# Optimization experiments

Measured on AMD Instinct MI355X. Metric: run time of the kernel, lower is better.

The kernel has to match this reference:

```python
import jax, jax.numpy as jnp
import numpy as np

B, T, C = 2, 2048, 512
H = 16
HS = C // H  # 32
DF = 4 * C   # 2048
EPS = 1e-3   # keras LayerNormalization default


def setup_inputs() -> dict:
    key = jax.random.key(0)
    ks = jax.random.split(key, 16)
    s = 0.02
    return {
        "x":  jax.random.normal(ks[0], (B, T, C), jnp.float32),
        "Wq": jax.random.normal(ks[1], (H, C, HS), jnp.float32) * s,
        "bq": jnp.zeros((H, HS), jnp.float32),
        "Wk": jax.random.normal(ks[2], (H, C, HS), jnp.float32) * s,
        "bk": jnp.zeros((H, HS), jnp.float32),
        "Wv": jax.random.normal(ks[3], (H, C, HS), jnp.float32) * s,
        "bv": jnp.zeros((H, HS), jnp.float32),
        "Wo": jax.random.normal(ks[4], (C, C), jnp.float32) * s,
        "bo": jnp.zeros((C,), jnp.float32),
        "W1": jax.random.normal(ks[5], (C, DF), jnp.float32) * s,
        "b1": jnp.zeros((DF,), jnp.float32),
        "W2": jax.random.normal(ks[6], (DF, C), jnp.float32) * s,
        "b2": jnp.zeros((C,), jnp.float32),
        "g1": jnp.ones((C,), jnp.float32),
        "be1": jnp.zeros((C,), jnp.float32),
        "g2": jnp.ones((C,), jnp.float32),
        "be2": jnp.zeros((C,), jnp.float32),
    }


def _layernorm(x, g, b):
    mu = jnp.mean(x, axis=-1, keepdims=True)
    var = jnp.mean(jnp.square(x - mu), axis=-1, keepdims=True)
    return (x - mu) / jnp.sqrt(var + EPS) * g + b


def reference(x, Wq, bq, Wk, bk, Wv, bv, Wo, bo, W1, b1, W2, b2, g1, be1, g2, be2):
    Bx, Tx, Cx = x.shape
    # --- attention branch (pre-LN) ---
    h = _layernorm(x, g1, be1)
    q = jnp.einsum('btc,hcd->bhtd', h, Wq) + bq[None, :, None, :]
    k = jnp.einsum('btc,hcd->bhtd', h, Wk) + bk[None, :, None, :]
    v = jnp.einsum('btc,hcd->bhtd', h, Wv) + bv[None, :, None, :]
    # NOTE: source code never applies 1/sqrt(head_size) to scores (mask-only scaling bug)
    scores = jnp.einsum('bhtd,bhsd->bhts', q, k)           # [B,H,T,T]
    causal = jnp.tril(jnp.ones((Tx, Tx), dtype=bool))
    scores = jnp.where(causal, scores, -jnp.inf)
    att = jax.nn.softmax(scores, axis=-1)
    o = jnp.einsum('bhts,bhsd->bhtd', att, v)              # [B,H,T,HS]
    o = o.transpose(0, 2, 1, 3).reshape(Bx, Tx, Cx)        # concat heads
    x = x + o @ Wo + bo
    # --- FFN branch (pre-LN) ---
    h2 = _layernorm(x, g2, be2)
    f = jax.nn.relu(h2 @ W1 + b1) @ W2 + b2
    return x + f
```

## Files before the change

kernel.cpp:

```cpp
#include <hip/hip_runtime.h>
#include <hip/hip_bf16.h>

#define T_  2048
#define C_  512
#define H_  16
#define HS_ 32
#define DF_ 2048
#define B_  2
#define M_  4096

typedef __attribute__((ext_vector_type(8))) short short8;
typedef __attribute__((ext_vector_type(4))) short short4v;
typedef __attribute__((ext_vector_type(4))) float f32x4;
typedef __attribute__((ext_vector_type(16))) float f32x16;

__device__ inline short bf16r(float f) {
  union { float f; unsigned u; } v; v.f = f;
  return (short)((v.u + 0x7FFFu + ((v.u >> 16) & 1u)) >> 16);
}

__device__ inline f32x4 mfma16(short8 a, short8 b, f32x4 c) {
  return __builtin_amdgcn_mfma_f32_16x16x32_bf16(a, b, c, 0, 0, 0);
}
__device__ inline f32x16 mfma32(short8 a, short8 b, f32x16 c) {
  return __builtin_amdgcn_mfma_f32_32x32x16_bf16(a, b, c, 0, 0, 0);
}

__device__ inline unsigned cvtpk(float lo, float hi) {
  unsigned r;
  asm("v_cvt_pk_bf16_f32 %0, %1, %2" : "=v"(r) : "v"(lo), "v"(hi));
  return r;
}

__device__ inline void gload_lds16(const short* g, short* l) {
  __builtin_amdgcn_global_load_lds(
      (const __attribute__((address_space(1))) unsigned int*)g,
      (__attribute__((address_space(3))) unsigned int*)l, 16, 0, 0);
}

__device__ inline void ln_row(int row, const float* src, const float* g,
                              const float* be, short* dst, int lane) {
  const float* xr = src + (size_t)row * C_;
  float4 a = *(const float4*)(xr + lane * 8);
  float4 b = *(const float4*)(xr + lane * 8 + 4);
  float vals[8] = {a.x, a.y, a.z, a.w, b.x, b.y, b.z, b.w};
  float s = 0.f, ss = 0.f;
  #pragma unroll
  for (int i = 0; i < 8; ++i) { s += vals[i]; ss += vals[i] * vals[i]; }
  #pragma unroll
  for (int off = 1; off < 64; off <<= 1) {
    s += __shfl_xor(s, off);
    ss += __shfl_xor(ss, off);
  }
  float mu = s * (1.f / C_);
  float rstd = rsqrtf(ss * (1.f / C_) - mu * mu + 1e-3f);
  short8 o;
  #pragma unroll
  for (int i = 0; i < 8; ++i)
    o[i] = bf16r((vals[i] - mu) * rstd * g[lane * 8 + i] + be[lane * 8 + i]);
  *(short8*)(dst + (size_t)row * C_ + lane * 8) = o;
}

__global__ __launch_bounds__(256) void prep_kernel(
    const float* __restrict__ x, const float* __restrict__ g1, const float* __restrict__ be1,
    const float* __restrict__ Wq, const float* __restrict__ Wk, const float* __restrict__ Wv,
    const float* __restrict__ Wo, const float* __restrict__ W1, const float* __restrict__ W2,
    short* __restrict__ h1, short* __restrict__ Wqkv, short* __restrict__ Wop,
    short* __restrict__ W1p, short* __restrict__ W2p) {
  __shared__ float tile[32][33];
  int id = blockIdx.x;
  int tid = threadIdx.x;
  if (id >= 3072) {
    int w = tid >> 6, lane = tid & 63;
    ln_row((id - 3072) * 4 + w, x, g1, be1, h1, lane);
    return;
  }
  const float* src; short* dst;
  int srcN, dstK, k0, n0;
  size_t dstBase;
  if (id < 768) {
    int s = id >> 4, ct = id & 15;
    int proj = s >> 4, hh = s & 15;
    src = (proj == 0 ? Wq : (proj == 1 ? Wk : Wv)) + (size_t)hh * 512 * 32;
    srcN = 32; dstK = 512; k0 = ct * 32; n0 = 0;
    dst = Wqkv; dstBase = (size_t)(proj * 512 + hh * 32);
  } else if (id < 1024) {
    int t = id - 768;
    src = Wo; srcN = 512; dstK = 512;
    k0 = (t >> 4) * 32; n0 = (t & 15) * 32; dst = Wop; dstBase = 0;
  } else if (id < 2048) {
    int t = id - 1024;
    src = W1; srcN = 2048; dstK = 512;
    k0 = (t >> 6) * 32; n0 = (t & 63) * 32; dst = W1p; dstBase = 0;
  } else {
    int t = id - 2048;
    src = W2; srcN = 512; dstK = 2048;
    k0 = (t >> 4) * 32; n0 = (t & 15) * 32; dst = W2p; dstBase = 0;
  }
  int rr = tid >> 3, rc = (tid & 7) * 4;
  float4 v4 = *(const float4*)(src + (size_t)(k0 + rr) * srcN + n0 + rc);
  tile[rr][rc + 0] = v4.x; tile[rr][rc + 1] = v4.y;
  tile[rr][rc + 2] = v4.z; tile[rr][rc + 3] = v4.w;
  __syncthreads();
  int wn = tid >> 3, wk = (tid & 7) * 4;
  short4v o;
  o[0] = bf16r(tile[wk + 0][wn]);
  o[1] = bf16r(tile[wk + 1][wn]);
  o[2] = bf16r(tile[wk + 2][wn]);
  o[3] = bf16r(tile[wk + 3][wn]);
  *(short4v*)(dst + (dstBase + n0 + wn) * (size_t)dstK + k0 + wk) = o;
}

__global__ __launch_bounds__(256) void ln2_kernel(
    const float* __restrict__ x, const float* __restrict__ g, const float* __restrict__ be,
    short* __restrict__ out) {
  int w = threadIdx.x >> 6, lane = threadIdx.x & 63;
  ln_row(blockIdx.x * 4 + w, x, g, be, out, lane);
}

template<int BM, int BN, int WM, int WN, int KDIM, int FM, int FN>
__device__ inline void gemm_core(const short* __restrict__ A, const short* __restrict__ Bw,
                                 int m0, int n0, f32x4 (&acc)[FM][FN]) {
  static_assert(WM * WN == 4 && FM == BM / WM / 16 && FN == BN / WN / 16, "geometry");
  __shared__ short lA[2][BM * 64];
  __shared__ short lB[2][BN * 64];
  const int tid = threadIdx.x, w = tid >> 6, lane = tid & 63;
  const int cl = lane & 15, g = lane >> 4;
  const int wm = w / WN, wn = w % WN;
  const int srow = tid >> 3;
  const int sug  = (tid & 7) ^ (srow & 7);
  constexpr int NT = KDIM / 64;

  auto stage = [&](int buf, int k0) {
    #pragma unroll
    for (int j = 0; j < BM / 32; ++j)
      gload_lds16(A + (size_t)(m0 + j * 32 + srow) * KDIM + k0 + sug * 8,
                  &lA[buf][j * 2048 + tid * 8]);
    #pragma unroll
    for (int j = 0; j < BN / 32; ++j)
      gload_lds16(Bw + (size_t)(n0 + j * 32 + srow) * KDIM + k0 + sug * 8,
                  &lB[buf][j * 2048 + tid * 8]);
  };

  stage(0, 0);
  __syncthreads();
  int cur = 0;
  for (int t = 0; t < NT; ++t) {
    if (t + 1 < NT) stage(cur ^ 1, (t + 1) * 64);
    #pragma unroll
    for (int kk = 0; kk < 2; ++kk) {
      const int uswz = ((kk * 4 + g) ^ (cl & 7)) * 8;
      short8 a[FM], b[FN];
      #pragma unroll
      for (int mi = 0; mi < FM; ++mi)
        a[mi] = *(const short8*)&lA[cur][(wm * (BM / WM) + mi * 16 + cl) * 64 + uswz];
      #pragma unroll
      for (int ni = 0; ni < FN; ++ni)
        b[ni] = *(const short8*)&lB[cur][(wn * (BN / WN) + ni * 16 + cl) * 64 + uswz];
      #pragma unroll
      for (int mi = 0; mi < FM; ++mi)
        #pragma unroll
        for (int ni = 0; ni < FN; ++ni)
          acc[mi][ni] = mfma16(a[mi], b[ni], acc[mi][ni]);
    }
    __syncthreads();
    cur ^= 1;
  }
}

__global__ __launch_bounds__(256) void gemm_qkvt(
    const short* __restrict__ h1, const short* __restrict__ Wqkv,
    const float* __restrict__ bq, const float* __restrict__ bk,
    const float* __restrict__ bv,
    short* __restrict__ qb, short* __restrict__ kb, short* __restrict__ vTb) {
  int id = blockIdx.x;
  const short *Ap, *Bp;
  int m0, n0;
  bool isv = id >= 512;
  if (!isv) { m0 = (id >> 3) * 64; n0 = (id & 7) * 128; Ap = h1; Bp = Wqkv; }
  else { int t = id - 512; m0 = (t & 7) * 64; n0 = (t >> 3) * 128;
         Ap = Wqkv + 1024 * 512; Bp = h1; }
  f32x4 acc[2][4] = {};
  gemm_core<64, 128, 2, 2, 512, 2, 4>(Ap, Bp, m0, n0, acc);
  int w = threadIdx.x >> 6, lane = threadIdx.x & 63;
  int cl = lane & 15, rb = (lane >> 4) * 4;
  int wm = w >> 1, wn = w & 1;
  if (!isv) {
    #pragma unroll
    for (int mi = 0; mi < 2; ++mi)
      #pragma unroll
      for (int ni = 0; ni < 4; ++ni)
        #pragma unroll
        for (int r = 0; r < 4; ++r) {
          int mm = m0 + wm * 32 + mi * 16 + rb + r;
          int n  = n0 + wn * 64 + ni * 16 + cl;
          int proj = n >> 9, rem = n & 511;
          int hh = rem >> 5, d = rem & 31;
          int b = mm >> 11, t = mm & (T_ - 1);
          size_t bh = (size_t)b * H_ + hh;
          float val = acc[mi][ni][r];
          if (proj == 0) qb[(bh * T_ + t) * HS_ + d] = bf16r(val + bq[rem]);
          else           kb[(bh * T_ + t) * HS_ + d] = bf16r(val + bk[rem]);
        }
  } else {
    #pragma unroll
    for (int mi = 0; mi < 2; ++mi)
      #pragma unroll
      for (int ni = 0; ni < 4; ++ni)
        #pragma unroll
        for (int r = 0; r < 4; ++r) {
          int m = m0 + wm * 32 + mi * 16 + rb + r;
          int n = n0 + wn * 64 + ni * 16 + cl;
          vTb[(size_t)(n >> 11) * (512 * 2048) + (size_t)m * T_ + (n & 2047)] =
              bf16r(acc[mi][ni][r] + bv[m]);
        }
  }
}

__global__ __launch_bounds__(256) void gemm_ffn1(
    const short* __restrict__ A, const short* __restrict__ W,
    const float* __restrict__ b1, short* __restrict__ f1) {
  int id = blockIdx.x;
  int xcd = id & 7, s = id >> 3;
  int m0 = (xcd * 8 + (s & 7)) * 64;
  int n0 = (s >> 3) * 128;
  f32x4 acc[2][4] = {};
  gemm_core<64, 128, 2, 2, 512, 2, 4>(A, W, m0, n0, acc);
  int w = threadIdx.x >> 6, lane = threadIdx.x & 63;
  int cl = lane & 15, rb = (lane >> 4) * 4;
  int wm = w >> 1, wn = w & 1;
  #pragma unroll
  for (int mi = 0; mi < 2; ++mi)
    #pragma unroll
    for (int ni = 0; ni < 4; ++ni)
      #pragma unroll
      for (int r = 0; r < 4; ++r) {
        int mm = m0 + wm * 32 + mi * 16 + rb + r;
        int n  = n0 + wn * 64 + ni * 16 + cl;
        f1[(size_t)mm * DF_ + n] = bf16r(fmaxf(acc[mi][ni][r] + b1[n], 0.f));
      }
}

template<int KDIM>
__global__ __launch_bounds__(256) void gemm_res(
    const short* __restrict__ A, const short* __restrict__ W,
    const float* __restrict__ bias, const float* __restrict__ res,
    float* __restrict__ dst) {
  __shared__ short lA[2][64 * 128];
  __shared__ short lB[2][64 * 128];
  int id = blockIdx.x;
  int xcd = id & 7, s = id >> 3;
  int m0 = (xcd * 8 + (s & 7)) * 64;
  int n0 = (s >> 3) * 64;
  const int tid = threadIdx.x, w = tid >> 6, lane = tid & 63;
  const int cl = lane & 15, g = lane >> 4;
  const int wm = w >> 1, wn = w & 1;
  const int srow16 = tid >> 4;
  const int sug = (tid & 15) ^ (srow16 & 7);
  constexpr int NT = KDIM / 128;
  f32x4 acc[2][2] = {};

  auto stage = [&](int buf, int k0) {
    #pragma unroll
    for (int j = 0; j < 4; ++j) {
      gload_lds16(A + (size_t)(m0 + j * 16 + srow16) * KDIM + k0 + sug * 8,
                  &lA[buf][j * 2048 + tid * 8]);
      gload_lds16(W + (size_t)(n0 + j * 16 + srow16) * KDIM + k0 + sug * 8,
                  &lB[buf][j * 2048 + tid * 8]);
    }
  };

  stage(0, 0);
  __syncthreads();
  int cur = 0;
  for (int t = 0; t < NT; ++t) {
    if (t + 1 < NT) stage(cur ^ 1, (t + 1) * 128);
    #pragma unroll
    for (int kk = 0; kk < 4; ++kk) {
      const int uswz = ((kk * 4 + g) ^ (cl & 7)) * 8;
      short8 a0 = *(const short8*)&lA[cur][(wm * 32 + cl) * 128 + uswz];
      short8 a1 = *(const short8*)&lA[cur][(wm * 32 + 16 + cl) * 128 + uswz];
      short8 b0 = *(const short8*)&lB[cur][(wn * 32 + cl) * 128 + uswz];
      short8 b1 = *(const short8*)&lB[cur][(wn * 32 + 16 + cl) * 128 + uswz];
      acc[0][0] = mfma16(a0, b0, acc[0][0]);
      acc[0][1] = mfma16(a0, b1, acc[0][1]);
      acc[1][0] = mfma16(a1, b0, acc[1][0]);
      acc[1][1] = mfma16(a1, b1, acc[1][1]);
    }
    __syncthreads();
    cur ^= 1;
  }

  int rb = (lane >> 4) * 4;
  #pragma unroll
  for (int mi = 0; mi < 2; ++mi)
    #pragma unroll
    for (int ni = 0; ni < 2; ++ni)
      #pragma unroll
      for (int r = 0; r < 4; ++r) {
        int mm = m0 + wm * 32 + mi * 16 + rb + r;
        int n  = n0 + wn * 32 + ni * 16 + cl;
        dst[(size_t)mm * C_ + n] = acc[mi][ni][r] + bias[n] + res[(size_t)mm * C_ + n];
      }
}

__global__ __launch_bounds__(256) void attn_kernel(
    const short* __restrict__ qb, const short* __restrict__ kb,
    const short* __restrict__ vTb, short* __restrict__ ob) {
  __shared__ float accbuf[4][64][17];
  __shared__ float lbuf[4][32];
  __shared__ short tbuf[32][34];
  const int id = blockIdx.x;
  const int xcd = id & 7, s = id >> 3;
  const int headin = s & 3;
  const int qt = 63 - (s >> 2);
  const int bh = xcd * 4 + headin;
  const int w = threadIdx.x >> 6, lane = threadIdx.x & 63;
  const int cl = lane & 31, g = lane >> 5;
  const int q0 = qt * 32, q = q0 + cl;
  const float L2E = 1.44269504f;
  const float NFM = -16.f * L2E;

  const short* Qp  = qb  + (size_t)bh * T_ * HS_;
  const short* Kp  = kb  + (size_t)bh * T_ * HS_;
  const short* VTp = vTb + (size_t)bh * HS_ * T_;

  const int nc   = (qt >> 1) + 1;
  const int cbeg = (nc * w) >> 2;
  const int cend = (nc * (w + 1)) >> 2;

  f32x16 acc = {};
  float l = 0.f;

  if (cbeg < cend) {
    short8 qf0 = *(const short8*)(Qp + (size_t)q * HS_ + g * 8);
    short8 qf1 = *(const short8*)(Qp + (size_t)q * HS_ + 16 + g * 8);

    for (int c = cbeg; c < cend; ++c) {
      const int kc = c << 6;
      short8 k00 = *(const short8*)(Kp + (size_t)(kc + cl) * HS_ + g * 8);
      short8 k01 = *(const short8*)(Kp + (size_t)(kc + cl) * HS_ + 16 + g * 8);
      short8 k10 = *(const short8*)(Kp + (size_t)(kc + 32 + cl) * HS_ + g * 8);
      short8 k11 = *(const short8*)(Kp + (size_t)(kc + 32 + cl) * HS_ + 16 + g * 8);
      short8 va = *(const short8*)(VTp + (size_t)cl * T_ + kc + g * 8);
      short8 vb = *(const short8*)(VTp + (size_t)cl * T_ + kc + 16 + g * 8);
      short8 vc = *(const short8*)(VTp + (size_t)cl * T_ + kc + 32 + g * 8);
      short8 vd = *(const short8*)(VTp + (size_t)cl * T_ + kc + 48 + g * 8);

      __builtin_amdgcn_s_setprio(1);
      f32x16 Z = {};
      f32x16 S0 = mfma32(k00, qf0, Z);
      S0 = mfma32(k01, qf1, S0);
      f32x16 S1 = mfma32(k10, qf0, Z);
      S1 = mfma32(k11, qf1, S1);
      __builtin_amdgcn_s_setprio(0);

      if (c == nc - 1) {
        #pragma unroll
        for (int r = 0; r < 16; ++r) {
          int key = kc + (r & 3) + 8 * (r >> 2) + 4 * g;
          if (key > q)      S0[r] = -1e30f;
          if (key + 32 > q) S1[r] = -1e30f;
        }
      }

      float p[32];
      #pragma unroll
      for (int r = 0; r < 16; ++r) {
        p[r]      = exp2f(fmaf(S0[r], L2E, NFM));
        p[16 + r] = exp2f(fmaf(S1[r], L2E, NFM));
      }
      float sm[8];
      #pragma unroll
      for (int r = 0; r < 8; ++r)
        sm[r] = (p[r] + p[r + 8]) + (p[16 + r] + p[24 + r]);
      #pragma unroll
      for (int r = 0; r < 4; ++r) sm[r] += sm[r + 4];
      float ps = (sm[0] + sm[1]) + (sm[2] + sm[3]);
      ps += __shfl_xor(ps, 32);
      l += ps;

      __builtin_amdgcn_s_setprio(1);
      #pragma unroll
      for (int sb = 0; sb < 4; ++sb) {
        unsigned L0 = cvtpk(p[sb * 8 + 0], p[sb * 8 + 1]);
        unsigned L1 = cvtpk(p[sb * 8 + 2], p[sb * 8 + 3]);
        unsigned H0 = cvtpk(p[sb * 8 + 4], p[sb * 8 + 5]);
        unsigned H1 = cvtpk(p[sb * 8 + 6], p[sb * 8 + 7]);
        auto r02 = __builtin_amdgcn_permlane32_swap(L0, H0, false, false);
        auto r13 = __builtin_amdgcn_permlane32_swap(L1, H1, false, false);
        union { unsigned u[4]; short8 v; } pb;
        pb.u[0] = r02[0]; pb.u[1] = r13[0]; pb.u[2] = r02[1]; pb.u[3] = r13[1];
        short8 vf = (sb == 0) ? va : (sb == 1) ? vb : (sb == 2) ? vc : vd;
        acc = mfma32(vf, pb.v, acc);
      }
      __builtin_amdgcn_s_setprio(0);
    }
  }

  #pragma unroll
  for (int r = 0; r < 16; ++r) accbuf[w][lane][r] = acc[r];
  if (lane < 32) lbuf[w][cl] = l;
  __syncthreads();

  if (w == 0) {
    float lsum = lbuf[0][cl] + lbuf[1][cl] + lbuf[2][cl] + lbuf[3][cl];
    float inv = 1.f / lsum;
    #pragma unroll
    for (int r = 0; r < 16; ++r) {
      float v = accbuf[0][lane][r] + accbuf[1][lane][r] +
                accbuf[2][lane][r] + accbuf[3][lane][r];
      int d = (r & 3) + 8 * (r >> 2) + 4 * g;
      tbuf[cl][d] = bf16r(v * inv);
    }
  }
  __syncthreads();

  int qr = threadIdx.x >> 3, col = (threadIdx.x & 7) * 4;
  const int b = bh >> 4, hh = bh & 15;
  short4v o4;
  o4[0] = tbuf[qr][col + 0];
  o4[1] = tbuf[qr][col + 1];
  o4[2] = tbuf[qr][col + 2];
  o4[3] = tbuf[qr][col + 3];
  *(short4v*)(ob + ((size_t)b * T_ + q0 + qr) * C_ + hh * HS_ + col) = o4;
}

#define OFF_H1   ((size_t)0)
#define OFF_WQKV ((size_t)4194304)
#define OFF_WO   ((size_t)5767168)
#define OFF_W1   ((size_t)6291456)
#define OFF_W2   ((size_t)8388608)
#define OFF_Q    ((size_t)10485760)
#define OFF_K    ((size_t)14680064)
#define OFF_VT   ((size_t)18874368)
#define OFF_O    ((size_t)23068672)
#define OFF_X1   ((size_t)27262976)
#define OFF_H2   ((size_t)35651584)
#define OFF_F1   ((size_t)39845888)

extern "C" void kernel_launch(void* const* d_in, const int* in_sizes, int n_in,
                              void* d_out, int out_size, void* d_ws, size_t ws_size,
                              hipStream_t stream) {
  const float* x   = (const float*)d_in[0];
  const float* Wq  = (const float*)d_in[1];
  const float* bq  = (const float*)d_in[2];
  const float* Wk  = (const float*)d_in[3];
  const float* bk  = (const float*)d_in[4];
  const float* Wv  = (const float*)d_in[5];
  const float* bv  = (const float*)d_in[6];
  const float* Wo  = (const float*)d_in[7];
  const float* bo  = (const float*)d_in[8];
  const float* W1  = (const float*)d_in[9];
  const float* b1  = (const float*)d_in[10];
  const float* W2  = (const float*)d_in[11];
  const float* b2  = (const float*)d_in[12];
  const float* g1  = (const float*)d_in[13];
  const float* be1 = (const float*)d_in[14];
  const float* g2  = (const float*)d_in[15];
  const float* be2 = (const float*)d_in[16];

  char* ws = (char*)d_ws;
  short* h1   = (short*)(ws + OFF_H1);
  short* Wqkv = (short*)(ws + OFF_WQKV);
  short* Wop  = (short*)(ws + OFF_WO);
  short* W1p  = (short*)(ws + OFF_W1);
  short* W2p  = (short*)(ws + OFF_W2);
  short* qb   = (short*)(ws + OFF_Q);
  short* kb   = (short*)(ws + OFF_K);
  short* vTb  = (short*)(ws + OFF_VT);
  short* ob   = (short*)(ws + OFF_O);
  float* x1   = (float*)(ws + OFF_X1);
  short* h2   = (short*)(ws + OFF_H2);
  short* f1   = (short*)(ws + OFF_F1);
  float* out  = (float*)d_out;

  prep_kernel<<<3072 + 1024, 256, 0, stream>>>(x, g1, be1, Wq, Wk, Wv, Wo, W1, W2,
                                               h1, Wqkv, Wop, W1p, W2p);
  gemm_qkvt<<<768, 256, 0, stream>>>(h1, Wqkv, bq, bk, bv, qb, kb, vTb);
  attn_kernel<<<2048, 256, 0, stream>>>(qb, kb, vTb, ob);
  gemm_res<512><<<512, 256, 0, stream>>>(ob, Wop, bo, x, x1);
  ln2_kernel<<<M_ / 4, 256, 0, stream>>>(x1, g2, be2, h2);
  gemm_ffn1<<<1024, 256, 0, stream>>>(h2, W1p, b1, f1);
  gemm_res<2048><<<512, 256, 0, stream>>>(f1, W2p, b2, x1, out);
}
```

Measured before the change: 103.3 us.

## Split-K the FFN2 GEMM with atomic accumulation into pre-initialized output

The second FFN GEMM (K=2048) is split four ways along K, running 2048 blocks instead of 512, and each block atomically adds its partial tile into the output. The LN2 kernel now also writes out = x1 + b2 so the atomics start from the residual plus bias. The goal is to fill more CUs in the last GEMM. In exchange it adds float atomic traffic and makes the summation order nondeterministic.

```diff
diff --git a/kernel.cpp b/kernel.cpp
--- a/kernel.cpp
+++ b/kernel.cpp
@@ -112,10 +112,37 @@
 }
 
 __global__ __launch_bounds__(256) void ln2_kernel(
-    const float* __restrict__ x, const float* __restrict__ g, const float* __restrict__ be,
-    short* __restrict__ out) {
+    const float* __restrict__ x1, const float* __restrict__ g, const float* __restrict__ be,
+    const float* __restrict__ b2, short* __restrict__ h2, float* __restrict__ outinit) {
   int w = threadIdx.x >> 6, lane = threadIdx.x & 63;
-  ln_row(blockIdx.x * 4 + w, x, g, be, out, lane);
+  int row = blockIdx.x * 4 + w;
+  const float* xr = x1 + (size_t)row * C_;
+  float4 a = *(const float4*)(xr + lane * 8);
+  float4 b = *(const float4*)(xr + lane * 8 + 4);
+  float vals[8] = {a.x, a.y, a.z, a.w, b.x, b.y, b.z, b.w};
+  float s = 0.f, ss = 0.f;
+  #pragma unroll
+  for (int i = 0; i < 8; ++i) { s += vals[i]; ss += vals[i] * vals[i]; }
+  #pragma unroll
+  for (int off = 1; off < 64; off <<= 1) {
+    s += __shfl_xor(s, off);
+    ss += __shfl_xor(ss, off);
+  }
+  float mu = s * (1.f / C_);
+  float rstd = rsqrtf(ss * (1.f / C_) - mu * mu + 1e-3f);
+  short8 o;
+  float4 i0, i1;
+  const float* b2p = b2 + lane * 8;
+  #pragma unroll
+  for (int i = 0; i < 8; ++i)
+    o[i] = bf16r((vals[i] - mu) * rstd * g[lane * 8 + i] + be[lane * 8 + i]);
+  i0.x = vals[0] + b2p[0]; i0.y = vals[1] + b2p[1];
+  i0.z = vals[2] + b2p[2]; i0.w = vals[3] + b2p[3];
+  i1.x = vals[4] + b2p[4]; i1.y = vals[5] + b2p[5];
+  i1.z = vals[6] + b2p[6]; i1.w = vals[7] + b2p[7];
+  *(short8*)(h2 + (size_t)row * C_ + lane * 8) = o;
+  *(float4*)(outinit + (size_t)row * C_ + lane * 8) = i0;
+  *(float4*)(outinit + (size_t)row * C_ + lane * 8 + 4) = i1;
 }
 
 template<int BM, int BN, int WM, int WN, int KDIM, int FM, int FN>
@@ -301,6 +328,69 @@
         int mm = m0 + wm * 32 + mi * 16 + rb + r;
         int n  = n0 + wn * 32 + ni * 16 + cl;
         dst[(size_t)mm * C_ + n] = acc[mi][ni][r] + bias[n] + res[(size_t)mm * C_ + n];
+      }
+}
+
+__global__ __launch_bounds__(256) void gemm_ffn2_sk(
+    const short* __restrict__ A, const short* __restrict__ W,
+    float* __restrict__ out) {
+  __shared__ short lA[2][64 * 128];
+  __shared__ short lB[2][64 * 128];
+  int id = blockIdx.x;
+  int xcd = id & 7, r2 = id >> 3;
+  int ks = r2 & 3, s = r2 >> 2;
+  int m0 = (xcd * 8 + (s & 7)) * 64;
+  int n0 = (s >> 3) * 64;
+  int kbase = ks * 512;
+  const int tid = threadIdx.x, w = tid >> 6, lane = tid & 63;
+  const int cl = lane & 15, g = lane >> 4;
+  const int wm = w >> 1, wn = w & 1;
+  const int srow16 = tid >> 4;
+  const int sug = (tid & 15) ^ (srow16 & 7);
+  constexpr int NT = 4;
+  f32x4 acc[2][2] = {};
+
+  auto stage = [&](int buf, int k0) {
+    #pragma unroll
+    for (int j = 0; j < 4; ++j) {
+      gload_lds16(A + (size_t)(m0 + j * 16 + srow16) * DF_ + kbase + k0 + sug * 8,
+                  &lA[buf][j * 2048 + tid * 8]);
+      gload_lds16(W + (size_t)(n0 + j * 16 + srow16) * DF_ + kbase + k0 + sug * 8,
+                  &lB[buf][j * 2048 + tid * 8]);
+    }
+  };
+
+  stage(0, 0);
+  __syncthreads();
+  int cur = 0;
+  for (int t = 0; t < NT; ++t) {
+    if (t + 1 < NT) stage(cur ^ 1, (t + 1) * 128);
+    #pragma unroll
+    for (int kk = 0; kk < 4; ++kk) {
+      const int uswz = ((kk * 4 + g) ^ (cl & 7)) * 8;
+      short8 a0 = *(const short8*)&lA[cur][(wm * 32 + cl) * 128 + uswz];
+      short8 a1 = *(const short8*)&lA[cur][(wm * 32 + 16 + cl) * 128 + uswz];
+      short8 b0 = *(const short8*)&lB[cur][(wn * 32 + cl) * 128 + uswz];
+      short8 b1 = *(const short8*)&lB[cur][(wn * 32 + 16 + cl) * 128 + uswz];
+      acc[0][0] = mfma16(a0, b0, acc[0][0]);
+      acc[0][1] = mfma16(a0, b1, acc[0][1]);
+      acc[1][0] = mfma16(a1, b0, acc[1][0]);
+      acc[1][1] = mfma16(a1, b1, acc[1][1]);
+    }
+    __syncthreads();
+    cur ^= 1;
+  }
+
+  int rb = (lane >> 4) * 4;
+  #pragma unroll
+  for (int mi = 0; mi < 2; ++mi)
+    #pragma unroll
+    for (int ni = 0; ni < 2; ++ni)
+      #pragma unroll
+      for (int r = 0; r < 4; ++r) {
+        int mm = m0 + wm * 32 + mi * 16 + rb + r;
+        int n  = n0 + wn * 32 + ni * 16 + cl;
+        atomicAdd(&out[(size_t)mm * C_ + n], acc[mi][ni][r]);
       }
 }
 
@@ -480,7 +570,7 @@
   gemm_qkvt<<<768, 256, 0, stream>>>(h1, Wqkv, bq, bk, bv, qb, kb, vTb);
   attn_kernel<<<2048, 256, 0, stream>>>(qb, kb, vTb, ob);
   gemm_res<512><<<512, 256, 0, stream>>>(ob, Wop, bo, x, x1);
-  ln2_kernel<<<M_ / 4, 256, 0, stream>>>(x1, g2, be2, h2);
+  ln2_kernel<<<M_ / 4, 256, 0, stream>>>(x1, g2, be2, b2, h2, out);
   gemm_ffn1<<<1024, 256, 0, stream>>>(h2, W1p, b1, f1);
-  gemm_res<2048><<<512, 256, 0, stream>>>(f1, W2p, b2, x1, out);
-}
+  gemm_ffn2_sk<<<2048, 256, 0, stream>>>(f1, W2p, out);
+}
```

New measurement: 123.0 us. +19.1%, slower.
